# Kernel optimization log

Measured on AMD Instinct MI355X. Metric: run time of the kernel, lower is better.

Reference implementation:

```python
import jax, jax.numpy as jnp
import numpy as np

EPS = 1e-06
NUM_HEADS = 16


def _rms_norm(x, g, eps=EPS):
    # normalize over the last (full model) dim, as WanRMSNorm(dim)
    var = jnp.mean(jnp.square(x), axis=-1, keepdims=True)
    return x * jax.lax.rsqrt(var + eps) * g


def _apply_rope(q, k, freqs):
    # q, k: [b, s, n, d]; freqs: [s, d//2] angles. Interleaved (complex) pairs
    b, s, n, d = q.shape
    cos = jnp.cos(freqs)[None, :, None, :]  # [1, s, 1, d//2]
    sin = jnp.sin(freqs)[None, :, None, :]

    def rot(t):
        tr = t.reshape(b, s, n, d // 2, 2)
        t0, t1 = tr[..., 0], tr[..., 1]
        o0 = t0 * cos - t1 * sin
        o1 = t0 * sin + t1 * cos
        return jnp.stack([o0, o1], axis=-1).reshape(b, s, n, d)

    return rot(q), rot(k)


def setup_inputs() -> dict:
    key = jax.random.key(0)
    ks = jax.random.split(key, 8)
    b, s, dim = 2, 2048, 2048
    hd = dim // NUM_HEADS
    x = jax.random.normal(ks[0], (b, s, dim), dtype=jnp.float32)
    seq_lens = jax.random.randint(ks[1], (b,), s // 2, s + 1, dtype=jnp.int32)
    grid_sizes = jax.random.randint(ks[2], (b, 3), 1, 16).astype(jnp.int64)
    freqs = jax.random.uniform(ks[3], (s, hd // 2), dtype=jnp.float32) * 6.283
    sc = 1.0 / np.sqrt(dim)
    Wq = jax.random.normal(ks[4], (dim, dim), dtype=jnp.float32) * sc
    Wk = jax.random.normal(ks[5], (dim, dim), dtype=jnp.float32) * sc
    Wv = jax.random.normal(ks[6], (dim, dim), dtype=jnp.float32) * sc
    Wo = jax.random.normal(ks[7], (dim, dim), dtype=jnp.float32) * sc
    bo = jnp.zeros((dim,), dtype=jnp.float32)
    gq = jnp.ones((dim,), dtype=jnp.float32)
    gk = jnp.ones((dim,), dtype=jnp.float32)
    return {"x": x, "seq_lens": seq_lens, "grid_sizes": grid_sizes, "freqs": freqs,
            "Wq": Wq, "Wk": Wk, "Wv": Wv, "Wo": Wo, "bo": bo, "gq": gq, "gk": gk}


def reference(x, seq_lens, grid_sizes, freqs, Wq, Wk, Wv, Wo, bo, gq, gk):
    b, s, dim = x.shape
    n = NUM_HEADS
    d = dim // n
    scale = d ** (-0.5)

    # QKV projections (Linear: x @ W.T), with RMSNorm over full dim on q/k
    q = _rms_norm(x @ Wq.T, gq).reshape(b, s, n, d)
    k = _rms_norm(x @ Wk.T, gk).reshape(b, s, n, d)
    v = (x @ Wv.T).reshape(b, s, n, d)

    q, k = _apply_rope(q, k, freqs)

    # varlen attention: keys beyond seq_lens[b] are masked out
    scores = jnp.einsum("bqnd,bknd->bnqk", q, k) * scale
    key_valid = jnp.arange(s)[None, None, None, :] < seq_lens[:, None, None, None]
    scores = jnp.where(key_valid, scores, jnp.float32(-1e9))
    probs = jax.nn.softmax(scores, axis=-1)
    attn = jnp.einsum("bnqk,bknd->bqnd", probs, v).reshape(b, s, dim)

    return attn @ Wo.T + bo
```

## Files before the change

kernel.cpp:

```cpp
#include <hip/hip_runtime.h>
#include <hip/hip_bf16.h>
#include <math.h>

#define BATCH 2
#define SEQ   2048
#define DIM   2048
#define NH    16
#define HD    128
#define NROWS (BATCH * SEQ)
#define EPS_RMS 1e-6f

typedef unsigned short ushort_t;
typedef unsigned int   uint_t;
typedef __bf16    bf16x8 __attribute__((ext_vector_type(8)));
typedef _Float16  f16x8  __attribute__((ext_vector_type(8)));
typedef float     f32x4  __attribute__((ext_vector_type(4)));

__device__ inline ushort_t f2bf(float f) {
    uint_t u = __builtin_bit_cast(uint_t, f);
    uint_t r = u + 0x7FFFu + ((u >> 16) & 1u);
    return (ushort_t)(r >> 16);
}
__device__ inline ushort_t f2h(float f) {
    return __builtin_bit_cast(ushort_t, (_Float16)f);
}

__global__ __launch_bounds__(256) void cvt_all_kernel(
    const float* __restrict__ x,  const float* __restrict__ wq,
    const float* __restrict__ wk, const float* __restrict__ wv,
    const float* __restrict__ wo,
    ushort_t* __restrict__ xh,  ushort_t* __restrict__ wqh,
    ushort_t* __restrict__ wkh, ushort_t* __restrict__ wvh,
    ushort_t* __restrict__ woh)
{
    const int blk = blockIdx.x;
    const float* src; ushort_t* dst; size_t base;
    if (blk < 4096) { src = x; dst = xh; base = (size_t)blk * 2048; }
    else {
        const int r = blk - 4096;
        const int wsel = r >> 11;
        base = (size_t)(r & 2047) * 2048;
        if      (wsel == 0) { src = wq; dst = wqh; }
        else if (wsel == 1) { src = wk; dst = wkh; }
        else if (wsel == 2) { src = wv; dst = wvh; }
        else                { src = wo; dst = woh; }
    }
    const size_t i = base + ((size_t)threadIdx.x << 3);
    float v[8];
    *(float4*)&v[0] = *(const float4*)&src[i];
    *(float4*)&v[4] = *(const float4*)&src[i + 4];
    uint_t pk[4];
#pragma unroll
    for (int j = 0; j < 4; ++j)
        pk[j] = (uint_t)f2h(v[2 * j]) | ((uint_t)f2h(v[2 * j + 1]) << 16);
    *(uint4*)&dst[i] = make_uint4(pk[0], pk[1], pk[2], pk[3]);
}

template<int MODE>
__global__ __launch_bounds__(256, 2) void gemm_f16_kernel(
    const ushort_t* __restrict__ Ah, const ushort_t* __restrict__ Bh,
    const float* __restrict__ bias,
    float* __restrict__ C, ushort_t* __restrict__ Ct,
    const int M, const int N, const int K)
{
    __shared__ __align__(16) ushort_t sA[4096], sB[4096];
    const int tid  = threadIdx.x;
    const int w    = tid >> 6;
    const int lane = tid & 63;
    const int m0 = blockIdx.y * 128;
    const int n0 = blockIdx.x * 128;

    const int scol = (lane & 3) << 3;
    const int wr = w >> 1, wc = w & 1;
    const int fr = lane & 15, quad = lane >> 4;

    f32x4 acc[4][4];
#pragma unroll
    for (int mi = 0; mi < 4; ++mi)
#pragma unroll
        for (int ni = 0; ni < 4; ++ni)
            acc[mi][ni] = (f32x4){0.f, 0.f, 0.f, 0.f};

    for (int k0 = 0; k0 < K; k0 += 32) {
        __syncthreads();
#pragma unroll
        for (int it = 0; it < 2; ++it) {
            const int row  = (w << 5) + (it << 4) + (lane >> 2);
            const int loff = (w << 10) + (it << 9);
            const size_t ga = (size_t)(m0 + row) * K + k0 + scol;
            const size_t gb = (size_t)(n0 + row) * K + k0 + scol;
            __builtin_amdgcn_global_load_lds(
                (const __attribute__((address_space(1))) uint_t*)(const void*)(Ah + ga),
                (__attribute__((address_space(3))) uint_t*)(void*)&sA[loff], 16, 0, 0);
            __builtin_amdgcn_global_load_lds(
                (const __attribute__((address_space(1))) uint_t*)(const void*)(Bh + gb),
                (__attribute__((address_space(3))) uint_t*)(void*)&sB[loff], 16, 0, 0);
        }
        __syncthreads();

        f16x8 bfr[4];
#pragma unroll
        for (int ni = 0; ni < 4; ++ni) {
            const int row = (wc << 6) + (ni << 4) + fr;
            bfr[ni] = *(const f16x8*)&sB[(row << 5) + (quad << 3)];
        }
#pragma unroll
        for (int mi = 0; mi < 4; ++mi) {
            const int row = (wr << 6) + (mi << 4) + fr;
            const f16x8 ah = *(const f16x8*)&sA[(row << 5) + (quad << 3)];
#pragma unroll
            for (int ni = 0; ni < 4; ++ni)
                acc[mi][ni] = __builtin_amdgcn_mfma_f32_16x16x32_f16(ah, bfr[ni], acc[mi][ni], 0, 0, 0);
        }
    }

#pragma unroll
    for (int mi = 0; mi < 4; ++mi)
#pragma unroll
        for (int ni = 0; ni < 4; ++ni) {
            const int col = n0 + (wc << 6) + (ni << 4) + fr;
            if (MODE == 0) {
                const float bv = bias ? bias[col] : 0.f;
#pragma unroll
                for (int r = 0; r < 4; ++r) {
                    const int rowg = m0 + (wr << 6) + (mi << 4) + (quad << 2) + r;
                    C[(size_t)rowg * N + col] = acc[mi][ni][r] + bv;
                }
            } else {
                const int rowg = m0 + (wr << 6) + (mi << 4) + (quad << 2);
                const int bb = rowg >> 11, tok = rowg & (SEQ - 1);
                const int hh = col >> 7, d = col & (HD - 1);
                uint2 pk;
                pk.x = (uint_t)f2bf(acc[mi][ni][0]) | ((uint_t)f2bf(acc[mi][ni][1]) << 16);
                pk.y = (uint_t)f2bf(acc[mi][ni][2]) | ((uint_t)f2bf(acc[mi][ni][3]) << 16);
                *(uint2*)&Ct[((size_t)(bb * NH + hh) * HD + d) * SEQ + tok] = pk;
            }
        }
}

#define BM 64
#define BN 64
#define BK 16

__global__ __launch_bounds__(256) void gemm_nt_kernel(
    const float* __restrict__ A, const float* __restrict__ W,
    const float* __restrict__ bias, float* __restrict__ C,
    const int M, const int N, const int K)
{
    __shared__ float As[BK][BM + 4];
    __shared__ float Bs[BK][BN + 4];
    const int tid = threadIdx.x;
    const int tx = tid & 15;
    const int ty = tid >> 4;
    const int m0 = blockIdx.y * BM;
    const int n0 = blockIdx.x * BN;
    const int ldr = tid >> 2;
    const int ldc = (tid & 3) << 2;

    float acc[4][4] = {};

    for (int k0 = 0; k0 < K; k0 += BK) {
        __syncthreads();
        const float4 av = *(const float4*)&A[(size_t)(m0 + ldr) * K + (k0 + ldc)];
        const float4 wv = *(const float4*)&W[(size_t)(n0 + ldr) * K + (k0 + ldc)];
        As[ldc + 0][ldr] = av.x; As[ldc + 1][ldr] = av.y;
        As[ldc + 2][ldr] = av.z; As[ldc + 3][ldr] = av.w;
        Bs[ldc + 0][ldr] = wv.x; Bs[ldc + 1][ldr] = wv.y;
        Bs[ldc + 2][ldr] = wv.z; Bs[ldc + 3][ldr] = wv.w;
        __syncthreads();
#pragma unroll
        for (int k = 0; k < BK; ++k) {
            const float4 a4 = *(const float4*)&As[k][ty << 2];
            const float4 b4 = *(const float4*)&Bs[k][tx << 2];
            const float aa[4] = {a4.x, a4.y, a4.z, a4.w};
            const float bb[4] = {b4.x, b4.y, b4.z, b4.w};
#pragma unroll
            for (int i = 0; i < 4; ++i)
#pragma unroll
                for (int j = 0; j < 4; ++j)
                    acc[i][j] = fmaf(aa[i], bb[j], acc[i][j]);
        }
    }

#pragma unroll
    for (int i = 0; i < 4; ++i) {
        const int row = m0 + (ty << 2) + i;
        const int col = n0 + (tx << 2);
        float4 ov;
        ov.x = acc[i][0]; ov.y = acc[i][1]; ov.z = acc[i][2]; ov.w = acc[i][3];
        if (bias != nullptr) {
            ov.x += bias[col + 0]; ov.y += bias[col + 1];
            ov.z += bias[col + 2]; ov.w += bias[col + 3];
        }
        *(float4*)&C[(size_t)row * N + col] = ov;
    }
}

__global__ __launch_bounds__(256) void rmsnorm_rope_qk_kernel(
    const float* __restrict__ Qb, const float* __restrict__ gq,
    ushort_t* __restrict__ qbh,
    const float* __restrict__ Kb, const float* __restrict__ gk,
    ushort_t* __restrict__ kbh,
    const float* __restrict__ freqs)
{
    const int r = blockIdx.x;
    const int s = r & (SEQ - 1);
    const int tid = threadIdx.x;
    const int base = tid << 3;
    const bool isQ = (blockIdx.y == 0);
    const float* T = isQ ? Qb : Kb;
    const float* g = isQ ? gq : gk;
    ushort_t* out  = isQ ? qbh : kbh;
    const float posc = isQ ? 0.088388347648318447f : 1.0f;

    float v[8];
    *(float4*)&v[0] = *(const float4*)&T[(size_t)r * DIM + base];
    *(float4*)&v[4] = *(const float4*)&T[(size_t)r * DIM + base + 4];

    float ss = 0.f;
#pragma unroll
    for (int i = 0; i < 8; ++i) ss += v[i] * v[i];
#pragma unroll
    for (int off = 32; off > 0; off >>= 1) ss += __shfl_down(ss, off);

    __shared__ float wsum[4];
    __shared__ float inv_sh;
    if ((tid & 63) == 0) wsum[tid >> 6] = ss;
    __syncthreads();
    if (tid == 0)
        inv_sh = rsqrtf((wsum[0] + wsum[1] + wsum[2] + wsum[3]) * (1.0f / DIM) + EPS_RMS);
    __syncthreads();
    const float inv = inv_sh * posc;

    float gg[8];
    *(float4*)&gg[0] = *(const float4*)&g[base];
    *(float4*)&gg[4] = *(const float4*)&g[base + 4];
#pragma unroll
    for (int i = 0; i < 8; ++i) v[i] *= inv * gg[i];

    const int p0 = (base & (HD - 1)) >> 1;
#pragma unroll
    for (int pp = 0; pp < 4; ++pp) {
        float sn, cs;
        __sincosf(freqs[(size_t)s * (HD / 2) + p0 + pp], &sn, &cs);
        const float t0 = v[2 * pp], t1 = v[2 * pp + 1];
        v[2 * pp]     = t0 * cs - t1 * sn;
        v[2 * pp + 1] = t0 * sn + t1 * cs;
    }

    uint_t pk[4];
#pragma unroll
    for (int j = 0; j < 4; ++j)
        pk[j] = (uint_t)f2bf(v[2 * j]) | ((uint_t)f2bf(v[2 * j + 1]) << 16);
    *(uint4*)&out[(size_t)r * DIM + base] = make_uint4(pk[0], pk[1], pk[2], pk[3]);
}

__global__ __launch_bounds__(256) void rmsnorm_rope_kernel(
    float* __restrict__ T, const float* __restrict__ g,
    const float* __restrict__ freqs)
{
    const int r = blockIdx.x;
    const int s = r & (SEQ - 1);
    const int tid = threadIdx.x;
    const int base = tid << 3;

    float v[8];
    *(float4*)&v[0] = *(const float4*)&T[(size_t)r * DIM + base];
    *(float4*)&v[4] = *(const float4*)&T[(size_t)r * DIM + base + 4];

    float ss = 0.f;
#pragma unroll
    for (int i = 0; i < 8; ++i) ss += v[i] * v[i];
#pragma unroll
    for (int off = 32; off > 0; off >>= 1) ss += __shfl_down(ss, off);

    __shared__ float wsum[4];
    __shared__ float inv_sh;
    if ((tid & 63) == 0) wsum[tid >> 6] = ss;
    __syncthreads();
    if (tid == 0)
        inv_sh = rsqrtf((wsum[0] + wsum[1] + wsum[2] + wsum[3]) * (1.0f / DIM) + EPS_RMS);
    __syncthreads();
    const float inv = inv_sh;

    float gg[8];
    *(float4*)&gg[0] = *(const float4*)&g[base];
    *(float4*)&gg[4] = *(const float4*)&g[base + 4];
#pragma unroll
    for (int i = 0; i < 8; ++i) v[i] *= inv * gg[i];

    const int p0 = (base & (HD - 1)) >> 1;
#pragma unroll
    for (int pp = 0; pp < 4; ++pp) {
        float sn, cs;
        __sincosf(freqs[(size_t)s * (HD / 2) + p0 + pp], &sn, &cs);
        const float t0 = v[2 * pp], t1 = v[2 * pp + 1];
        v[2 * pp]     = t0 * cs - t1 * sn;
        v[2 * pp + 1] = t0 * sn + t1 * cs;
    }

    *(float4*)&T[(size_t)r * DIM + base]     = *(float4*)&v[0];
    *(float4*)&T[(size_t)r * DIM + base + 4] = *(float4*)&v[4];
}

#define AQ 128
#define AK 64
#define KSTR 136
#define VSTR 72

__global__ __launch_bounds__(256, 2) void attn_mfma_kernel(
    const ushort_t* __restrict__ QH, const ushort_t* __restrict__ KH,
    const ushort_t* __restrict__ VtG, const int* __restrict__ seq_lens,
    ushort_t* __restrict__ Oh)
{
    __shared__ __align__(16) ushort_t sK[AK * KSTR];
    __shared__ __align__(16) ushort_t sVt[HD * VSTR];
    __shared__ __align__(16) ushort_t sP[AQ * VSTR];

    const int tid  = threadIdx.x;
    const int w    = tid >> 6;
    const int lane = tid & 63;
    const int fr   = lane & 15;
    const int quad = lane >> 4;
    const int q0   = blockIdx.x * AQ;
    const int h    = blockIdx.y;
    const int b    = blockIdx.z;
    const int len  = seq_lens[b];

    bf16x8 qfrag[2][4];
#pragma unroll
    for (int qt = 0; qt < 2; ++qt)
#pragma unroll
        for (int h4 = 0; h4 < 4; ++h4) {
            const size_t qrow = (size_t)(b * SEQ + q0 + (w << 5) + (qt << 4) + fr);
            qfrag[qt][h4] = *(const bf16x8*)&QH[qrow * DIM + h * HD + (h4 << 5) + (quad << 3)];
        }

    f32x4 Oacc[2][8];
#pragma unroll
    for (int qt = 0; qt < 2; ++qt)
#pragma unroll
        for (int dt = 0; dt < 8; ++dt)
            Oacc[qt][dt] = (f32x4){0.f, 0.f, 0.f, 0.f};
    float mrow[2] = {-1.0e30f, -1.0e30f};
    float lrow[2] = {0.f, 0.f};

    const int ntiles = (len + AK - 1) / AK;
    for (int t = 0; t < ntiles; ++t) {
        const int k0 = t * AK;
        const bool masked = (k0 + AK > len);
        __syncthreads();
        for (int i = tid; i < AK * 16; i += 256) {
            const int key = i >> 4, c8 = (i & 15) << 3;
            const uint4 kv = *(const uint4*)&KH[(size_t)(b * SEQ + k0 + key) * DIM + h * HD + c8];
            *(uint4*)&sK[key * KSTR + c8] = kv;
        }
        for (int i = tid; i < HD * 8; i += 256) {
            const int d = i >> 3, kc = (i & 7) << 3;
            const uint4 vv = *(const uint4*)&VtG[((size_t)(b * NH + h) * HD + d) * SEQ + k0 + kc];
            *(uint4*)&sVt[d * VSTR + kc] = vv;
        }
        __syncthreads();

        f32x4 S[4][2];
#pragma unroll
        for (int kt = 0; kt < 4; ++kt) {
            bf16x8 kf[4];
#pragma unroll
            for (int h4 = 0; h4 < 4; ++h4)
                kf[h4] = *(const bf16x8*)&sK[((kt << 4) + fr) * KSTR + (h4 << 5) + (quad << 3)];
#pragma unroll
            for (int qt = 0; qt < 2; ++qt) {
                f32x4 a = (f32x4){0.f, 0.f, 0.f, 0.f};
#pragma unroll
                for (int h4 = 0; h4 < 4; ++h4)
                    a = __builtin_amdgcn_mfma_f32_16x16x32_bf16(kf[h4], qfrag[qt][h4], a, 0, 0, 0);
                S[kt][qt] = a;
            }
        }

#pragma unroll
        for (int qt = 0; qt < 2; ++qt) {
            float tm = -1.0e30f;
            if (masked) {
#pragma unroll
                for (int kt = 0; kt < 4; ++kt)
#pragma unroll
                    for (int r = 0; r < 4; ++r) {
                        const int key = k0 + (kt << 4) + (quad << 2) + r;
                        float s = (key < len) ? S[kt][qt][r] : -1.0e30f;
                        S[kt][qt][r] = s;
                        tm = fmaxf(tm, s);
                    }
            } else {
#pragma unroll
                for (int kt = 0; kt < 4; ++kt)
#pragma unroll
                    for (int r = 0; r < 4; ++r)
                        tm = fmaxf(tm, S[kt][qt][r]);
            }
            tm = fmaxf(tm, __shfl_xor(tm, 16));
            tm = fmaxf(tm, __shfl_xor(tm, 32));
            const float mnew = fmaxf(mrow[qt], tm);
            const float alpha = __expf(mrow[qt] - mnew);
            mrow[qt] = mnew;
            float rsum = 0.f;
#pragma unroll
            for (int kt = 0; kt < 4; ++kt) {
                float p[4];
#pragma unroll
                for (int r = 0; r < 4; ++r) {
                    p[r] = __expf(S[kt][qt][r] - mnew);
                    rsum += p[r];
                }
                uint2 pk;
                pk.x = (uint_t)f2bf(p[0]) | ((uint_t)f2bf(p[1]) << 16);
                pk.y = (uint_t)f2bf(p[2]) | ((uint_t)f2bf(p[3]) << 16);
                *(uint2*)&sP[((w << 5) + (qt << 4) + fr) * VSTR + (kt << 4) + (quad << 2)] = pk;
            }
            rsum += __shfl_xor(rsum, 16);
            rsum += __shfl_xor(rsum, 32);
            lrow[qt] = lrow[qt] * alpha + rsum;
#pragma unroll
            for (int r = 0; r < 4; ++r) {
                const float ar = __shfl(alpha, (quad << 2) + r);
#pragma unroll
                for (int dt = 0; dt < 8; ++dt)
                    Oacc[qt][dt][r] *= ar;
            }
        }

#pragma unroll
        for (int ks = 0; ks < 2; ++ks) {
            bf16x8 pf[2];
#pragma unroll
            for (int qt = 0; qt < 2; ++qt)
                pf[qt] = *(const bf16x8*)&sP[((w << 5) + (qt << 4) + fr) * VSTR + (ks << 5) + (quad << 3)];
#pragma unroll
            for (int dt = 0; dt < 8; ++dt) {
                const bf16x8 vf = *(const bf16x8*)&sVt[((dt << 4) + fr) * VSTR + (ks << 5) + (quad << 3)];
#pragma unroll
                for (int qt = 0; qt < 2; ++qt)
                    Oacc[qt][dt] = __builtin_amdgcn_mfma_f32_16x16x32_bf16(pf[qt], vf, Oacc[qt][dt], 0, 0, 0);
            }
        }
    }

#pragma unroll
    for (int qt = 0; qt < 2; ++qt) {
        float linv[4];
#pragma unroll
        for (int r = 0; r < 4; ++r)
            linv[r] = 1.0f / __shfl(lrow[qt], (quad << 2) + r);
#pragma unroll
        for (int dt = 0; dt < 8; ++dt)
#pragma unroll
            for (int r = 0; r < 4; ++r) {
                const int qrow = q0 + (w << 5) + (qt << 4) + (quad << 2) + r;
                Oh[(size_t)(b * SEQ + qrow) * DIM + h * HD + (dt << 4) + fr] =
                    f2h(Oacc[qt][dt][r] * linv[r]);
            }
    }
}

#define BQ  64
#define BKT 64

__global__ __launch_bounds__(256) void attn_kernel(
    const float* __restrict__ Q, const float* __restrict__ K,
    const float* __restrict__ V, const int* __restrict__ seq_lens,
    float* __restrict__ O)
{
    const int qt = blockIdx.x;
    const int h  = blockIdx.y;
    const int b  = blockIdx.z;
    const int len = seq_lens[b];
    const int q0 = qt * BQ;
    const float scale = 0.088388347648318447f;

    __shared__ float Qst[HD][BQ + 4];
    __shared__ float Kst[HD][BKT + 4];
    __shared__ float Vs[BKT][HD + 4];
    __shared__ float Sc[BQ][BKT + 1];
    __shared__ float mrow[BQ], lrow[BQ], alpha_s[BQ];

    const int tid = threadIdx.x;
    const int si0 = (tid >> 4) << 2;
    const int sj0 = (tid & 15) << 2;
    const int pi0 = (tid >> 4) << 2;
    const int pc0 = (tid & 15) << 3;

    for (int i = tid; i < BQ * HD / 4; i += 256) {
        const int e = i << 2;
        const int row = e >> 7;
        const int c0 = e & (HD - 1);
        const float4 qv = *(const float4*)&Q[(size_t)(b * SEQ + q0 + row) * DIM + h * HD + c0];
        Qst[c0 + 0][row] = qv.x; Qst[c0 + 1][row] = qv.y;
        Qst[c0 + 2][row] = qv.z; Qst[c0 + 3][row] = qv.w;
    }
    if (tid < BQ) { mrow[tid] = -3.0e38f; lrow[tid] = 0.f; }

    float o[4][8] = {};
    __syncthreads();

    const int ntiles = (len + BKT - 1) / BKT;
    for (int t = 0; t < ntiles; ++t) {
        const int k0 = t * BKT;
        __syncthreads();
        for (int i = tid; i < BKT * HD / 4; i += 256) {
            const int e = i << 2;
            const int row = e >> 7;
            const int c0 = e & (HD - 1);
            const int kg = k0 + row;
            float4 kv = make_float4(0.f, 0.f, 0.f, 0.f);
            float4 vv = make_float4(0.f, 0.f, 0.f, 0.f);
            if (kg < len) {
                kv = *(const float4*)&K[(size_t)(b * SEQ + kg) * DIM + h * HD + c0];
                vv = *(const float4*)&V[(size_t)(b * SEQ + kg) * DIM + h * HD + c0];
            }
            Kst[c0 + 0][row] = kv.x; Kst[c0 + 1][row] = kv.y;
            Kst[c0 + 2][row] = kv.z; Kst[c0 + 3][row] = kv.w;
            *(float4*)&Vs[row][c0] = vv;
        }
        __syncthreads();

        float acc[4][4] = {};
#pragma unroll 8
        for (int kk = 0; kk < HD; ++kk) {
            const float4 q4 = *(const float4*)&Qst[kk][si0];
            const float4 k4 = *(const float4*)&Kst[kk][sj0];
            const float qa[4] = {q4.x, q4.y, q4.z, q4.w};
            const float ka[4] = {k4.x, k4.y, k4.z, k4.w};
#pragma unroll
            for (int i = 0; i < 4; ++i)
#pragma unroll
                for (int j = 0; j < 4; ++j)
                    acc[i][j] = fmaf(qa[i], ka[j], acc[i][j]);
        }
#pragma unroll
        for (int i = 0; i < 4; ++i)
#pragma unroll
            for (int j = 0; j < 4; ++j) {
                const int jg = k0 + sj0 + j;
                Sc[si0 + i][sj0 + j] = (jg < len) ? acc[i][j] * scale : -1.0e9f;
            }
        __syncthreads();

        if (tid < BQ) {
            const int i = tid;
            const float m_old = mrow[i];
            float mx = m_old;
            for (int j = 0; j < BKT; ++j) mx = fmaxf(mx, Sc[i][j]);
            const float al = __expf(m_old - mx);
            float sum = 0.f;
            for (int j = 0; j < BKT; ++j) {
                const float p = __expf(Sc[i][j] - mx);
                Sc[i][j] = p;
                sum += p;
            }
            mrow[i] = mx;
            lrow[i] = lrow[i] * al + sum;
            alpha_s[i] = al;
        }
        __syncthreads();

#pragma unroll
        for (int i = 0; i < 4; ++i) {
            const float al = alpha_s[pi0 + i];
#pragma unroll
            for (int c = 0; c < 8; ++c) o[i][c] *= al;
        }
        for (int j = 0; j < BKT; ++j) {
            float p[4];
#pragma unroll
            for (int i = 0; i < 4; ++i) p[i] = Sc[pi0 + i][j];
            const float4 v0 = *(const float4*)&Vs[j][pc0];
            const float4 v1 = *(const float4*)&Vs[j][pc0 + 4];
            const float va[8] = {v0.x, v0.y, v0.z, v0.w, v1.x, v1.y, v1.z, v1.w};
#pragma unroll
            for (int i = 0; i < 4; ++i)
#pragma unroll
                for (int c = 0; c < 8; ++c)
                    o[i][c] = fmaf(p[i], va[c], o[i][c]);
        }
    }

#pragma unroll
    for (int i = 0; i < 4; ++i) {
        const float invl = 1.0f / lrow[pi0 + i];
        float4 w0, w1;
        w0.x = o[i][0] * invl; w0.y = o[i][1] * invl;
        w0.z = o[i][2] * invl; w0.w = o[i][3] * invl;
        w1.x = o[i][4] * invl; w1.y = o[i][5] * invl;
        w1.z = o[i][6] * invl; w1.w = o[i][7] * invl;
        float* op = &O[(size_t)(b * SEQ + q0 + pi0 + i) * DIM + h * HD + pc0];
        *(float4*)&op[0] = w0;
        *(float4*)&op[4] = w1;
    }
}

extern "C" void kernel_launch(void* const* d_in, const int* in_sizes, int n_in,
                              void* d_out, int out_size, void* d_ws, size_t ws_size,
                              hipStream_t stream)
{
    const float* x        = (const float*)d_in[0];
    const int*   seq_lens = (const int*)d_in[1];
    const float* freqs    = (const float*)d_in[3];
    const float* Wq       = (const float*)d_in[4];
    const float* Wk       = (const float*)d_in[5];
    const float* Wv       = (const float*)d_in[6];
    const float* Wo       = (const float*)d_in[7];
    const float* bo       = (const float*)d_in[8];
    const float* gq       = (const float*)d_in[9];
    const float* gk       = (const float*)d_in[10];
    float* out = (float*)d_out;

    const size_t mat = (size_t)NROWS * DIM;
    const size_t wsz = (size_t)DIM * DIM;

    float*    Qb   = (float*)d_ws;
    float*    Kb   = Qb + mat;
    ushort_t* xh   = (ushort_t*)(Kb + mat);
    ushort_t* wqh  = xh + mat;
    ushort_t* wkh  = wqh + wsz;
    ushort_t* wvh  = wkh + wsz;
    ushort_t* woh  = wvh + wsz;
    ushort_t* qbh  = woh + wsz;
    ushort_t* kbh  = qbh + mat;
    ushort_t* vtg  = kbh + mat;
    ushort_t* abh  = vtg + mat;

    const size_t need = 2 * mat * sizeof(float)
                      + (mat + 4 * wsz + 4 * mat) * sizeof(ushort_t);

    if (ws_size >= need) {
        cvt_all_kernel<<<12288, 256, 0, stream>>>(
            x, Wq, Wk, Wv, Wo, xh, wqh, wkh, wvh, woh);

        const dim3 gg(DIM / 128, NROWS / 128);
        gemm_f16_kernel<0><<<gg, 256, 0, stream>>>(xh, wqh, nullptr, Qb, nullptr, NROWS, DIM, DIM);
        gemm_f16_kernel<0><<<gg, 256, 0, stream>>>(xh, wkh, nullptr, Kb, nullptr, NROWS, DIM, DIM);
        gemm_f16_kernel<1><<<gg, 256, 0, stream>>>(xh, wvh, nullptr, nullptr, vtg, NROWS, DIM, DIM);

        rmsnorm_rope_qk_kernel<<<dim3(NROWS, 2), 256, 0, stream>>>(
            Qb, gq, qbh, Kb, gk, kbh, freqs);

        attn_mfma_kernel<<<dim3(SEQ / AQ, NH, BATCH), 256, 0, stream>>>(qbh, kbh, vtg, seq_lens, abh);

        gemm_f16_kernel<0><<<gg, 256, 0, stream>>>(abh, woh, bo, out, nullptr, NROWS, DIM, DIM);
    } else {
        float* Vb = Kb + mat;
        float* Ab = Vb + mat;
        const dim3 gemm_grid(DIM / BN, NROWS / BM);
        gemm_nt_kernel<<<gemm_grid, 256, 0, stream>>>(x, Wq, nullptr, Qb, NROWS, DIM, DIM);
        gemm_nt_kernel<<<gemm_grid, 256, 0, stream>>>(x, Wk, nullptr, Kb, NROWS, DIM, DIM);
        gemm_nt_kernel<<<gemm_grid, 256, 0, stream>>>(x, Wv, nullptr, Vb, NROWS, DIM, DIM);
        rmsnorm_rope_kernel<<<NROWS, 256, 0, stream>>>(Qb, gq, freqs);
        rmsnorm_rope_kernel<<<NROWS, 256, 0, stream>>>(Kb, gk, freqs);
        attn_kernel<<<dim3(SEQ / BQ, NH, BATCH), 256, 0, stream>>>(Qb, Kb, Vb, seq_lens, Ab);
        gemm_nt_kernel<<<gemm_grid, 256, 0, stream>>>(Ab, Wo, bo, out, NROWS, DIM, DIM);
    }
}
```

Baseline: 518.8 us.

## Fuse QKV GEMMs with direct-to-LDS loads; lazy softmax rescale and MFMA priority

Replaces the three separate Q/K/V projection launches with one 1536-block kernel. It picks the weight matrix per block, remaps block IDs for L2 locality and loads tiles with global_load_lds straight into shared memory. In attention, the online softmax skips rescaling O and l unless the row max rises by more than a threshold, and MFMA sections are wrapped in s_setprio raises. The lazy rescale lets exponentials reach up to e^8 before normalization, which trades some precision headroom for fewer multiplies and shuffles.

```diff
diff --git a/kernel.cpp b/kernel.cpp
--- a/kernel.cpp
+++ b/kernel.cpp
@@ -138,6 +138,99 @@
         }
 }
 
+__global__ __launch_bounds__(256, 3) void qkv_gemm_kernel(
+    const ushort_t* __restrict__ Ah, const ushort_t* __restrict__ Bq,
+    const ushort_t* __restrict__ Bk, const ushort_t* __restrict__ Bv,
+    float* __restrict__ Qb, float* __restrict__ Kb, ushort_t* __restrict__ Vt)
+{
+    __shared__ __align__(16) ushort_t sA[4096], sB[4096];
+    const int tid  = threadIdx.x;
+    const int w    = tid >> 6;
+    const int lane = tid & 63;
+
+    const int bid = blockIdx.x;
+    const int nid = (bid & 7) * 192 + (bid >> 3);
+    const int n_blk = nid >> 5;
+    const int m_blk = nid & 31;
+    const int wsel  = n_blk >> 4;
+    const int m0 = m_blk * 128;
+    const int n0 = (n_blk & 15) * 128;
+    const ushort_t* __restrict__ Bh = (wsel == 0) ? Bq : (wsel == 1) ? Bk : Bv;
+
+    const int scol = (lane & 3) << 3;
+    const int wr = w >> 1, wc = w & 1;
+    const int fr = lane & 15, quad = lane >> 4;
+
+    f32x4 acc[4][4];
+#pragma unroll
+    for (int mi = 0; mi < 4; ++mi)
+#pragma unroll
+        for (int ni = 0; ni < 4; ++ni)
+            acc[mi][ni] = (f32x4){0.f, 0.f, 0.f, 0.f};
+
+    for (int k0 = 0; k0 < DIM; k0 += 32) {
+        __syncthreads();
+#pragma unroll
+        for (int it = 0; it < 2; ++it) {
+            const int row  = (w << 5) + (it << 4) + (lane >> 2);
+            const int loff = (w << 10) + (it << 9);
+            const size_t ga = (size_t)(m0 + row) * DIM + k0 + scol;
+            const size_t gb = (size_t)(n0 + row) * DIM + k0 + scol;
+            __builtin_amdgcn_global_load_lds(
+                (const __attribute__((address_space(1))) uint_t*)(const void*)(Ah + ga),
+                (__attribute__((address_space(3))) uint_t*)(void*)&sA[loff], 16, 0, 0);
+            __builtin_amdgcn_global_load_lds(
+                (const __attribute__((address_space(1))) uint_t*)(const void*)(Bh + gb),
+                (__attribute__((address_space(3))) uint_t*)(void*)&sB[loff], 16, 0, 0);
+        }
+        __syncthreads();
+
+        f16x8 bfr[4];
+#pragma unroll
+        for (int ni = 0; ni < 4; ++ni) {
+            const int row = (wc << 6) + (ni << 4) + fr;
+            bfr[ni] = *(const f16x8*)&sB[(row << 5) + (quad << 3)];
+        }
+#pragma unroll
+        for (int mi = 0; mi < 4; ++mi) {
+            const int row = (wr << 6) + (mi << 4) + fr;
+            const f16x8 ah = *(const f16x8*)&sA[(row << 5) + (quad << 3)];
+#pragma unroll
+            for (int ni = 0; ni < 4; ++ni)
+                acc[mi][ni] = __builtin_amdgcn_mfma_f32_16x16x32_f16(ah, bfr[ni], acc[mi][ni], 0, 0, 0);
+        }
+    }
+
+    if (wsel < 2) {
+        float* __restrict__ C = (wsel == 0) ? Qb : Kb;
+#pragma unroll
+        for (int mi = 0; mi < 4; ++mi)
+#pragma unroll
+            for (int ni = 0; ni < 4; ++ni) {
+                const int col = n0 + (wc << 6) + (ni << 4) + fr;
+#pragma unroll
+                for (int r = 0; r < 4; ++r) {
+                    const int rowg = m0 + (wr << 6) + (mi << 4) + (quad << 2) + r;
+                    C[(size_t)rowg * DIM + col] = acc[mi][ni][r];
+                }
+            }
+    } else {
+#pragma unroll
+        for (int mi = 0; mi < 4; ++mi)
+#pragma unroll
+            for (int ni = 0; ni < 4; ++ni) {
+                const int col = n0 + (wc << 6) + (ni << 4) + fr;
+                const int rowg = m0 + (wr << 6) + (mi << 4) + (quad << 2);
+                const int bb = rowg >> 11, tok = rowg & (SEQ - 1);
+                const int hh = col >> 7, d = col & (HD - 1);
+                uint2 pk;
+                pk.x = (uint_t)f2bf(acc[mi][ni][0]) | ((uint_t)f2bf(acc[mi][ni][1]) << 16);
+                pk.y = (uint_t)f2bf(acc[mi][ni][2]) | ((uint_t)f2bf(acc[mi][ni][3]) << 16);
+                *(uint2*)&Vt[((size_t)(bb * NH + hh) * HD + d) * SEQ + tok] = pk;
+            }
+    }
+}
+
 #define BM 64
 #define BN 64
 #define BK 16
@@ -307,6 +400,7 @@
 #define AK 64
 #define KSTR 136
 #define VSTR 72
+#define RESCALE_THR 8.0f
 
 __global__ __launch_bounds__(256, 2) void attn_mfma_kernel(
     const ushort_t* __restrict__ QH, const ushort_t* __restrict__ KH,
@@ -363,6 +457,7 @@
         __syncthreads();
 
         f32x4 S[4][2];
+        __builtin_amdgcn_s_setprio(1);
 #pragma unroll
         for (int kt = 0; kt < 4; ++kt) {
             bf16x8 kf[4];
@@ -378,6 +473,7 @@
                 S[kt][qt] = a;
             }
         }
+        __builtin_amdgcn_s_setprio(0);
 
 #pragma unroll
         for (int qt = 0; qt < 2; ++qt) {
@@ -401,9 +497,24 @@
             }
             tm = fmaxf(tm, __shfl_xor(tm, 16));
             tm = fmaxf(tm, __shfl_xor(tm, 32));
-            const float mnew = fmaxf(mrow[qt], tm);
-            const float alpha = __expf(mrow[qt] - mnew);
-            mrow[qt] = mnew;
+
+            float mnew;
+            if (__all(tm - mrow[qt] <= RESCALE_THR)) {
+                mnew = mrow[qt];
+            } else {
+                mnew = fmaxf(mrow[qt], tm);
+                const float alpha = __expf(mrow[qt] - mnew);
+                mrow[qt] = mnew;
+                lrow[qt] *= alpha;
+#pragma unroll
+                for (int r = 0; r < 4; ++r) {
+                    const float ar = __shfl(alpha, (quad << 2) + r);
+#pragma unroll
+                    for (int dt = 0; dt < 8; ++dt)
+                        Oacc[qt][dt][r] *= ar;
+                }
+            }
+
             float rsum = 0.f;
 #pragma unroll
             for (int kt = 0; kt < 4; ++kt) {
@@ -420,16 +531,10 @@
             }
             rsum += __shfl_xor(rsum, 16);
             rsum += __shfl_xor(rsum, 32);
-            lrow[qt] = lrow[qt] * alpha + rsum;
-#pragma unroll
-            for (int r = 0; r < 4; ++r) {
-                const float ar = __shfl(alpha, (quad << 2) + r);
-#pragma unroll
-                for (int dt = 0; dt < 8; ++dt)
-                    Oacc[qt][dt][r] *= ar;
-            }
-        }
-
+            lrow[qt] += rsum;
+        }
+
+        __builtin_amdgcn_s_setprio(1);
 #pragma unroll
         for (int ks = 0; ks < 2; ++ks) {
             bf16x8 pf[2];
@@ -444,6 +549,7 @@
                     Oacc[qt][dt] = __builtin_amdgcn_mfma_f32_16x16x32_bf16(pf[qt], vf, Oacc[qt][dt], 0, 0, 0);
             }
         }
+        __builtin_amdgcn_s_setprio(0);
     }
 
 #pragma unroll
@@ -637,16 +743,14 @@
         cvt_all_kernel<<<12288, 256, 0, stream>>>(
             x, Wq, Wk, Wv, Wo, xh, wqh, wkh, wvh, woh);
 
-        const dim3 gg(DIM / 128, NROWS / 128);
-        gemm_f16_kernel<0><<<gg, 256, 0, stream>>>(xh, wqh, nullptr, Qb, nullptr, NROWS, DIM, DIM);
-        gemm_f16_kernel<0><<<gg, 256, 0, stream>>>(xh, wkh, nullptr, Kb, nullptr, NROWS, DIM, DIM);
-        gemm_f16_kernel<1><<<gg, 256, 0, stream>>>(xh, wvh, nullptr, nullptr, vtg, NROWS, DIM, DIM);
+        qkv_gemm_kernel<<<1536, 256, 0, stream>>>(xh, wqh, wkh, wvh, Qb, Kb, vtg);
 
         rmsnorm_rope_qk_kernel<<<dim3(NROWS, 2), 256, 0, stream>>>(
             Qb, gq, qbh, Kb, gk, kbh, freqs);
 
         attn_mfma_kernel<<<dim3(SEQ / AQ, NH, BATCH), 256, 0, stream>>>(qbh, kbh, vtg, seq_lens, abh);
 
+        const dim3 gg(DIM / 128, NROWS / 128);
         gemm_f16_kernel<0><<<gg, 256, 0, stream>>>(abh, woh, bo, out, nullptr, NROWS, DIM, DIM);
     } else {
         float* Vb = Kb + mat;
```

Measured after the change: 512.0 us. No clear change (-1.3%).
